# Kernel tuning notes

Hardware: AMD Instinct MI355X
Metric: run time of the kernel (lower is better)

Reference implementation:

```python
import jax, jax.numpy as jnp
import numpy as np

TAU = 0.01
MASK_VALUE = -1000000.0


def setup_inputs() -> dict:
    key = jax.random.key(0)
    kq, kk, km, k1, k2, k3 = jax.random.split(key, 6)
    B, Lq, Lk = 4, 512, 512
    Dq = Dk = 256
    H = 128
    queries = jax.random.normal(kq, (B, Lq, Dq), dtype=jnp.float32)
    keys = jax.random.normal(kk, (B, Lk, Dk), dtype=jnp.float32)
    # valid length along the size-2 logits axis, in {1, 2}
    mask = jax.random.randint(km, (B, Lq, Lk), 1, 3, dtype=jnp.int32)
    Wq = jax.random.normal(k1, (H, Dq), dtype=jnp.float32) * 0.05
    Wk = jax.random.normal(k2, (H, Dk), dtype=jnp.float32) * 0.05
    Wv = jax.random.normal(k3, (2, H), dtype=jnp.float32) * 0.05
    return {"queries": queries, "keys": keys, "mask": mask,
            "Wq": Wq, "Wk": Wk, "Wv": Wv}


def reference(queries, keys, mask, Wq, Wk, Wv):
    # Linear projections (no bias): [B,Lq,H], [B,Lk,H]
    q = jnp.einsum('bqd,hd->bqh', queries, Wq)
    k = jnp.einsum('bkd,hd->bkh', keys, Wk)
    # Bahdanau broadcast-add + tanh: [B,Lq,Lk,H]
    features = jnp.tanh(q[:, :, None, :] + k[:, None, :, :])
    # Project to 2 logits: [B,Lq,Lk,2]
    scores = jnp.einsum('bqkh,ch->bqkc', features, Wv)
    # sequence_mask along the size-2 last axis: positions >= valid_len get -1e6
    pos = jnp.arange(2, dtype=mask.dtype)
    masked = jnp.where(pos < mask[..., None], scores, MASK_VALUE)
    # Gumbel-softmax (soft), tau=0.01, over last axis; take channel 0
    g = jax.random.gumbel(jax.random.key(42), masked.shape, dtype=masked.dtype)
    weights = jax.nn.softmax((masked + g) / TAU, axis=-1)
    return weights[..., 0]
```

## Files before the change

### kernel.cpp

```cpp
#include <hip/hip_runtime.h>
#include <stdint.h>


#define BB 4
#define LLEN 512
#define DD 256
#define HH 128

#define TWO_LOG2E 2.8853900817779268f
#define LOG2E_100 144.26950408889634f

__device__ __forceinline__ uint32_t rotl32(uint32_t v, int r) {
  return __builtin_amdgcn_alignbit(v, v, 32 - r);
}

__device__ __forceinline__ void tf4_round(uint32_t x0[4], uint32_t x1[4],
                                          const int r) {
  #pragma unroll
  for (int i = 0; i < 4; ++i) {
    x0[i] += x1[i];
    x1[i] = rotl32(x1[i], r);
    x1[i] ^= x0[i];
  }
}
__device__ __forceinline__ void tf4_key(uint32_t x0[4], uint32_t x1[4],
                                        const uint32_t a, const uint32_t b) {
  #pragma unroll
  for (int i = 0; i < 4; ++i) { x0[i] += a; x1[i] += b; }
}

__device__ __forceinline__ void tf2x32_x4(const uint32_t c[4], uint32_t o[4]) {
  const uint32_t k0 = 0u;
  const uint32_t k1 = 42u;
  const uint32_t k2 = 0x1BD11BDAu ^ k0 ^ k1;

  uint32_t x0[4], x1[4];
  #pragma unroll
  for (int i = 0; i < 4; ++i) { x0[i] = k0; x1[i] = c[i] + k1; }

  tf4_round(x0, x1, 13); tf4_round(x0, x1, 15);
  tf4_round(x0, x1, 26); tf4_round(x0, x1, 6);
  tf4_key(x0, x1, k1, k2 + 1u);
  tf4_round(x0, x1, 17); tf4_round(x0, x1, 29);
  tf4_round(x0, x1, 16); tf4_round(x0, x1, 24);
  tf4_key(x0, x1, k2, k0 + 2u);
  tf4_round(x0, x1, 13); tf4_round(x0, x1, 15);
  tf4_round(x0, x1, 26); tf4_round(x0, x1, 6);
  tf4_key(x0, x1, k0, k1 + 3u);
  tf4_round(x0, x1, 17); tf4_round(x0, x1, 29);
  tf4_round(x0, x1, 16); tf4_round(x0, x1, 24);
  tf4_key(x0, x1, k1, k2 + 4u);
  tf4_round(x0, x1, 13); tf4_round(x0, x1, 15);
  tf4_round(x0, x1, 26); tf4_round(x0, x1, 6);
  tf4_key(x0, x1, k2, k0 + 5u);

  #pragma unroll
  for (int i = 0; i < 4; ++i) o[i] = x0[i] ^ x1[i];
}

__device__ __forceinline__ float u01_from_bits(uint32_t bits) {
  const float f = __uint_as_float((bits >> 9) | 0x3F800000u) - 1.0f;
  return fmaxf(f, 1.17549435e-38f);
}

__global__ __launch_bounds__(128) void proj_kernel(
    const float* __restrict__ queries, const float* __restrict__ keys,
    const float* __restrict__ Wq, const float* __restrict__ Wk,
    float* __restrict__ EQ, float* __restrict__ EK) {
  const int blk = blockIdx.x;
  const bool isK = blk >= 512;
  const int rb = (isK ? blk - 512 : blk) * 4;
  const float* __restrict__ in = isK ? keys : queries;
  const float* __restrict__ W  = isK ? Wk : Wq;
  float* __restrict__ outp     = isK ? EK : EQ;

  __shared__ float rows[4][DD];
  const float4* in4 = reinterpret_cast<const float4*>(in + (size_t)rb * DD);
  float4* rows4 = reinterpret_cast<float4*>(&rows[0][0]);
  #pragma unroll
  for (int t = threadIdx.x; t < 4 * DD / 4; t += 128) rows4[t] = in4[t];
  __syncthreads();

  const int h = threadIdx.x;
  const float4* W4 = reinterpret_cast<const float4*>(W + (size_t)h * DD);
  float a0 = 0.f, a1 = 0.f, a2 = 0.f, a3 = 0.f;
  #pragma unroll 8
  for (int d4 = 0; d4 < DD / 4; ++d4) {
    const float4 w = W4[d4];
    const int d = d4 * 4;
    a0 = fmaf(w.x, rows[0][d], fmaf(w.y, rows[0][d+1], fmaf(w.z, rows[0][d+2], fmaf(w.w, rows[0][d+3], a0))));
    a1 = fmaf(w.x, rows[1][d], fmaf(w.y, rows[1][d+1], fmaf(w.z, rows[1][d+2], fmaf(w.w, rows[1][d+3], a1))));
    a2 = fmaf(w.x, rows[2][d], fmaf(w.y, rows[2][d+1], fmaf(w.z, rows[2][d+2], fmaf(w.w, rows[2][d+3], a2))));
    a3 = fmaf(w.x, rows[3][d], fmaf(w.y, rows[3][d+1], fmaf(w.z, rows[3][d+2], fmaf(w.w, rows[3][d+3], a3))));
  }
  float* orow = outp + (size_t)rb * HH + h;
  orow[0 * HH] = __builtin_amdgcn_exp2f(a0 * TWO_LOG2E);
  orow[1 * HH] = __builtin_amdgcn_exp2f(a1 * TWO_LOG2E);
  orow[2 * HH] = __builtin_amdgcn_exp2f(a2 * TWO_LOG2E);
  orow[3 * HH] = __builtin_amdgcn_exp2f(a3 * TWO_LOG2E);
}

#define GRP(accv, qv, kv, wd) {                                       \
    float4 A_;                                                        \
    A_.x = fmaf((qv).x, (kv).x, 1.0f);                                \
    A_.y = fmaf((qv).y, (kv).y, 1.0f);                                \
    A_.z = fmaf((qv).z, (kv).z, 1.0f);                                \
    A_.w = fmaf((qv).w, (kv).w, 1.0f);                                \
    const float p01_ = A_.x * A_.y;                                   \
    const float p23_ = A_.z * A_.w;                                   \
    const float n01_ = fmaf((wd).x, A_.y, (wd).y * A_.x);             \
    const float n23_ = fmaf((wd).z, A_.w, (wd).w * A_.z);             \
    const float num_ = fmaf(n01_, p23_, n23_ * p01_);                 \
    const float rc_  = __builtin_amdgcn_rcpf(p01_ * p23_);            \
    (accv) = fmaf(num_, rc_, (accv)); }

__global__ __launch_bounds__(256) void attn_kernel(
    const float* __restrict__ EQ, const float* __restrict__ EK,
    const int* __restrict__ mask, const float* __restrict__ Wv,
    float* __restrict__ out) {
  __shared__ float4 QL[32][33];
  __shared__ float4 KL[64][33];
  __shared__ float4 wdL[32];

  const int bi = blockIdx.x, bj = blockIdx.y, b = blockIdx.z;
  const int i0 = bi * 32, j0 = bj * 64;

  const float4* Q4 = reinterpret_cast<const float4*>(EQ) + ((size_t)b * LLEN + i0) * (HH / 4);
  const float4* K4 = reinterpret_cast<const float4*>(EK) + ((size_t)b * LLEN + j0) * (HH / 4);
  for (int t = threadIdx.x; t < 1024 + 2048; t += 256) {
    if (t < 1024) {
      QL[t >> 5][t & 31] = Q4[t];
    } else {
      const int u = t - 1024;
      KL[u >> 5][u & 31] = K4[u];
    }
  }
  if (threadIdx.x < 32) {
    const float4 w0 = reinterpret_cast<const float4*>(Wv)[threadIdx.x];
    const float4 w1 = reinterpret_cast<const float4*>(Wv)[32 + threadIdx.x];
    float4 wd; wd.x = w0.x - w1.x; wd.y = w0.y - w1.y;
    wd.z = w0.z - w1.z; wd.w = w0.w - w1.w;
    wdL[threadIdx.x] = wd;
  }
  __syncthreads();

  const int jj = threadIdx.x & 31;
  const int ib = threadIdx.x >> 5;

  const uint32_t row0 = (uint32_t)b * LLEN + i0 + ib;
  const uint32_t col0 = j0 + jj;
  int mreg[4][2];
  #pragma unroll
  for (int r = 0; r < 4; ++r)
    #pragma unroll
    for (int c = 0; c < 2; ++c)
      mreg[r][c] = mask[(row0 + 8u * r) * LLEN + col0 + 32u * c];

  float Swd = 0.f;
  #pragma unroll
  for (int t = 0; t < 32; ++t) {
    const float4 wd = wdL[t];
    Swd += (wd.x + wd.y) + (wd.z + wd.w);
  }

  float acc[4][2] = {{0.f,0.f},{0.f,0.f},{0.f,0.f},{0.f,0.f}};

  #pragma unroll 4
  for (int h4 = 0; h4 < HH / 4; ++h4) {
    const float4 kv0 = KL[jj][h4];
    const float4 kv1 = KL[jj + 32][h4];
    const float4 wd  = wdL[h4];
    const float4 qv0 = QL[ib][h4];
    const float4 qv1 = QL[ib + 8][h4];
    const float4 qv2 = QL[ib + 16][h4];
    const float4 qv3 = QL[ib + 24][h4];
    GRP(acc[0][0], qv0, kv0, wd) GRP(acc[0][1], qv0, kv1, wd)
    GRP(acc[1][0], qv1, kv0, wd) GRP(acc[1][1], qv1, kv1, wd)
    GRP(acc[2][0], qv2, kv0, wd) GRP(acc[2][1], qv2, kv1, wd)
    GRP(acc[3][0], qv3, kv0, wd) GRP(acc[3][1], qv3, kv1, wd)
  }

  #pragma unroll
  for (int half = 0; half < 2; ++half) {
    uint32_t idx[4];
    float    dv[4];
    int      mm[4];
    #pragma unroll
    for (int k = 0; k < 4; ++k) {
      const int r = half * 2 + (k >> 1);
      const int c = k & 1;
      idx[k] = (row0 + 8u * r) * LLEN + col0 + 32u * c;
      dv[k]  = fmaf(-2.0f, acc[r][c], Swd);
      mm[k]  = mreg[r][c];
    }

    uint32_t c0[4], c1[4];
    #pragma unroll
    for (int k = 0; k < 4; ++k) { c0[k] = idx[k] * 2u; c1[k] = idx[k] * 2u + 1u; }
    uint32_t b0[4], b1[4];
    tf2x32_x4(c0, b0);
    tf2x32_x4(c1, b1);

    #pragma unroll
    for (int k = 0; k < 4; ++k) {
      const float l0 = __log2f(u01_from_bits(b0[k]));
      const float l1 = __log2f(u01_from_bits(b1[k]));
      const float rl = l1 * __builtin_amdgcn_rcpf(l0);
      const float g_ = 100.0f * __log2f(rl);
      const float t_ = fmaf(dv[k], LOG2E_100, g_);
      const float o_ = __builtin_amdgcn_rcpf(1.0f + __builtin_amdgcn_exp2f(-t_));
      out[idx[k]] = (mm[k] >= 2) ? o_ : 1.0f;
    }
  }
}

extern "C" void kernel_launch(void* const* d_in, const int* in_sizes, int n_in,
                              void* d_out, int out_size, void* d_ws, size_t ws_size,
                              hipStream_t stream) {
  const float* queries = (const float*)d_in[0];
  const float* keys    = (const float*)d_in[1];
  const int*   mask    = (const int*)d_in[2];
  const float* Wq      = (const float*)d_in[3];
  const float* Wk      = (const float*)d_in[4];
  const float* Wv      = (const float*)d_in[5];
  float* out = (float*)d_out;

  float* EQ = (float*)d_ws;
  float* EK = EQ + (size_t)BB * LLEN * HH;

  proj_kernel<<<dim3(1024), dim3(128), 0, stream>>>(
      queries, keys, Wq, Wk, EQ, EK);
  attn_kernel<<<dim3(LLEN / 32, LLEN / 64, BB), dim3(256), 0, stream>>>(
      EQ, EK, mask, Wv, out);
}
```

Measured before the change: 43.85 us.

## Split hidden-dim reduction in halves and move Gumbel epilogue to separate kernel

The attention kernel now splits the 128-wide hidden reduction into two halves on separate blocks, doubling the grid. Each half writes a partial logit difference to a workspace buffer. A new elementwise epilogue kernel sums the two partials, generates the threefry Gumbel noise, applies the mask and writes the output with vectorised loads and stores. The aim is more parallelism and less register pressure in the main loop. The cost is an extra kernel launch and a round trip of two 1M-float partial buffers through global memory.

```diff
diff --git a/kernel.cpp b/kernel.cpp
--- a/kernel.cpp
+++ b/kernel.cpp
@@ -9,6 +9,8 @@
 
 #define TWO_LOG2E 2.8853900817779268f
 #define LOG2E_100 144.26950408889634f
+
+#define NSITES (BB * LLEN * LLEN)
 
 __device__ __forceinline__ uint32_t rotl32(uint32_t v, int r) {
   return __builtin_amdgcn_alignbit(v, v, 32 - r);
@@ -114,25 +116,28 @@
     const float rc_  = __builtin_amdgcn_rcpf(p01_ * p23_);            \
     (accv) = fmaf(num_, rc_, (accv)); }
 
-__global__ __launch_bounds__(256) void attn_kernel(
+__global__ __launch_bounds__(256) void attn_loop(
     const float* __restrict__ EQ, const float* __restrict__ EK,
-    const int* __restrict__ mask, const float* __restrict__ Wv,
-    float* __restrict__ out) {
-  __shared__ float4 QL[32][33];
-  __shared__ float4 KL[64][33];
+    const float* __restrict__ Wv, float* __restrict__ pbuf) {
+  __shared__ float4 QL[32][17];
+  __shared__ float4 KL[64][17];
   __shared__ float4 wdL[32];
 
-  const int bi = blockIdx.x, bj = blockIdx.y, b = blockIdx.z;
+  const int bi = blockIdx.x, bj = blockIdx.y;
+  const int b = blockIdx.z >> 1, half = blockIdx.z & 1;
   const int i0 = bi * 32, j0 = bj * 64;
+  const int h4b = half * 16;
 
   const float4* Q4 = reinterpret_cast<const float4*>(EQ) + ((size_t)b * LLEN + i0) * (HH / 4);
   const float4* K4 = reinterpret_cast<const float4*>(EK) + ((size_t)b * LLEN + j0) * (HH / 4);
-  for (int t = threadIdx.x; t < 1024 + 2048; t += 256) {
-    if (t < 1024) {
-      QL[t >> 5][t & 31] = Q4[t];
+  for (int t = threadIdx.x; t < 512 + 1024; t += 256) {
+    if (t < 512) {
+      const int row = t >> 4, hh = t & 15;
+      QL[row][hh] = Q4[row * (HH / 4) + h4b + hh];
     } else {
-      const int u = t - 1024;
-      KL[u >> 5][u & 31] = K4[u];
+      const int u = t - 512;
+      const int row = u >> 4, hh = u & 15;
+      KL[row][hh] = K4[row * (HH / 4) + h4b + hh];
     }
   }
   if (threadIdx.x < 32) {
@@ -147,29 +152,21 @@
   const int jj = threadIdx.x & 31;
   const int ib = threadIdx.x >> 5;
 
-  const uint32_t row0 = (uint32_t)b * LLEN + i0 + ib;
-  const uint32_t col0 = j0 + jj;
-  int mreg[4][2];
-  #pragma unroll
-  for (int r = 0; r < 4; ++r)
-    #pragma unroll
-    for (int c = 0; c < 2; ++c)
-      mreg[r][c] = mask[(row0 + 8u * r) * LLEN + col0 + 32u * c];
-
   float Swd = 0.f;
   #pragma unroll
   for (int t = 0; t < 32; ++t) {
     const float4 wd = wdL[t];
     Swd += (wd.x + wd.y) + (wd.z + wd.w);
   }
+  const float base = half ? 0.0f : Swd;
 
   float acc[4][2] = {{0.f,0.f},{0.f,0.f},{0.f,0.f},{0.f,0.f}};
 
   #pragma unroll 4
-  for (int h4 = 0; h4 < HH / 4; ++h4) {
+  for (int h4 = 0; h4 < 16; ++h4) {
     const float4 kv0 = KL[jj][h4];
     const float4 kv1 = KL[jj + 32][h4];
-    const float4 wd  = wdL[h4];
+    const float4 wd  = wdL[h4b + h4];
     const float4 qv0 = QL[ib][h4];
     const float4 qv1 = QL[ib + 8][h4];
     const float4 qv2 = QL[ib + 16][h4];
@@ -180,38 +177,60 @@
     GRP(acc[3][0], qv3, kv0, wd) GRP(acc[3][1], qv3, kv1, wd)
   }
 
-  #pragma unroll
-  for (int half = 0; half < 2; ++half) {
-    uint32_t idx[4];
-    float    dv[4];
-    int      mm[4];
+  float* __restrict__ pb = pbuf + (size_t)half * NSITES;
+  const uint32_t row0 = (uint32_t)b * LLEN + i0 + ib;
+  const uint32_t col0 = j0 + jj;
+  #pragma unroll
+  for (int r = 0; r < 4; ++r) {
     #pragma unroll
-    for (int k = 0; k < 4; ++k) {
-      const int r = half * 2 + (k >> 1);
-      const int c = k & 1;
-      idx[k] = (row0 + 8u * r) * LLEN + col0 + 32u * c;
-      dv[k]  = fmaf(-2.0f, acc[r][c], Swd);
-      mm[k]  = mreg[r][c];
+    for (int c = 0; c < 2; ++c) {
+      const uint32_t idx = (row0 + 8u * r) * LLEN + col0 + 32u * c;
+      pb[idx] = fmaf(-2.0f, acc[r][c], base);
     }
-
-    uint32_t c0[4], c1[4];
-    #pragma unroll
-    for (int k = 0; k < 4; ++k) { c0[k] = idx[k] * 2u; c1[k] = idx[k] * 2u + 1u; }
-    uint32_t b0[4], b1[4];
-    tf2x32_x4(c0, b0);
-    tf2x32_x4(c1, b1);
-
-    #pragma unroll
-    for (int k = 0; k < 4; ++k) {
-      const float l0 = __log2f(u01_from_bits(b0[k]));
-      const float l1 = __log2f(u01_from_bits(b1[k]));
-      const float rl = l1 * __builtin_amdgcn_rcpf(l0);
-      const float g_ = 100.0f * __log2f(rl);
-      const float t_ = fmaf(dv[k], LOG2E_100, g_);
-      const float o_ = __builtin_amdgcn_rcpf(1.0f + __builtin_amdgcn_exp2f(-t_));
-      out[idx[k]] = (mm[k] >= 2) ? o_ : 1.0f;
-    }
-  }
+  }
+}
+
+__global__ __launch_bounds__(256) void attn_epi(
+    const float* __restrict__ pA, const float* __restrict__ pB,
+    const int* __restrict__ mask, float* __restrict__ out) {
+  const uint32_t t4 = (uint32_t)blockIdx.x * 256u + threadIdx.x;
+  const uint32_t s0 = t4 * 4u;
+
+  const float4 a = reinterpret_cast<const float4*>(pA)[t4];
+  const float4 bv = reinterpret_cast<const float4*>(pB)[t4];
+  const int4  m  = reinterpret_cast<const int4*>(mask)[t4];
+
+  float dv[4];
+  dv[0] = a.x + bv.x; dv[1] = a.y + bv.y;
+  dv[2] = a.z + bv.z; dv[3] = a.w + bv.w;
+
+  uint32_t c0[4], c1[4];
+  #pragma unroll
+  for (int k = 0; k < 4; ++k) {
+    c0[k] = (s0 + (uint32_t)k) * 2u;
+    c1[k] = (s0 + (uint32_t)k) * 2u + 1u;
+  }
+  uint32_t b0[4], b1[4];
+  tf2x32_x4(c0, b0);
+  tf2x32_x4(c1, b1);
+
+  float o[4];
+  #pragma unroll
+  for (int k = 0; k < 4; ++k) {
+    const float l0 = __log2f(u01_from_bits(b0[k]));
+    const float l1 = __log2f(u01_from_bits(b1[k]));
+    const float rl = l1 * __builtin_amdgcn_rcpf(l0);
+    const float g_ = 100.0f * __log2f(rl);
+    const float t_ = fmaf(dv[k], LOG2E_100, g_);
+    o[k] = __builtin_amdgcn_rcpf(1.0f + __builtin_amdgcn_exp2f(-t_));
+  }
+
+  float4 res;
+  res.x = (m.x >= 2) ? o[0] : 1.0f;
+  res.y = (m.y >= 2) ? o[1] : 1.0f;
+  res.z = (m.z >= 2) ? o[2] : 1.0f;
+  res.w = (m.w >= 2) ? o[3] : 1.0f;
+  reinterpret_cast<float4*>(out)[t4] = res;
 }
 
 extern "C" void kernel_launch(void* const* d_in, const int* in_sizes, int n_in,
@@ -225,11 +244,14 @@
   const float* Wv      = (const float*)d_in[5];
   float* out = (float*)d_out;
 
-  float* EQ = (float*)d_ws;
-  float* EK = EQ + (size_t)BB * LLEN * HH;
+  float* EQ   = (float*)d_ws;
+  float* EK   = EQ + (size_t)BB * LLEN * HH;
+  float* pbuf = EK + (size_t)BB * LLEN * HH;
 
   proj_kernel<<<dim3(1024), dim3(128), 0, stream>>>(
       queries, keys, Wq, Wk, EQ, EK);
-  attn_kernel<<<dim3(LLEN / 32, LLEN / 64, BB), dim3(256), 0, stream>>>(
-      EQ, EK, mask, Wv, out);
-}
+  attn_loop<<<dim3(LLEN / 32, LLEN / 64, 2 * BB), dim3(256), 0, stream>>>(
+      EQ, EK, Wv, pbuf);
+  attn_epi<<<dim3(NSITES / 4 / 256), dim3(256), 0, stream>>>(
+      pbuf, pbuf + NSITES, mask, out);
+}
```

After: 47.57 us. 8.5% more time.
